# Kernel tuning notes

Hardware: AMD Instinct MI355X
Metric: run time of the kernel (lower is better)

## Reference

```python
import jax, jax.numpy as jnp
import numpy as np

N_NODES = 100000
N_EDGES = 1600000
N_GRAPHS = 64
D_IN, D_HID, D_OUT = 256, 128, 64
EPS = 1e-5


def gcn_conv(x, edge_index, edge_weight, W, b):
    """PyG GCNConv: add_self_loops=True, normalize=True (sym deg norm), bias."""
    n = x.shape[0]
    row = jnp.concatenate([edge_index[0], jnp.arange(n)])      # source
    col = jnp.concatenate([edge_index[1], jnp.arange(n)])      # target
    w = jnp.concatenate([edge_weight, jnp.ones((n,), x.dtype)])
    deg = jax.ops.segment_sum(w, col, num_segments=n)
    dinv = jnp.where(deg > 0, jax.lax.rsqrt(jnp.maximum(deg, EPS)), 0.0)
    norm = dinv[row] * w * dinv[col]                           # [E+N]
    h = x @ W                                                  # [N, out]
    msg = h[row] * norm[:, None]                               # [E+N, out]
    out = jax.ops.segment_sum(msg, col, num_segments=n)
    return out + b


def layer_norm(x, gamma, beta):
    mu = jnp.mean(x, axis=-1, keepdims=True)
    var = jnp.mean(jnp.square(x - mu), axis=-1, keepdims=True)
    return (x - mu) * jax.lax.rsqrt(var + EPS) * gamma + beta


def setup_inputs() -> dict:
    key = jax.random.key(0)
    ks = jax.random.split(key, 12)
    x = jax.random.normal(ks[0], (N_NODES, D_IN), jnp.float32)
    edge_index = jax.random.randint(ks[1], (2, N_EDGES), 0, N_NODES, jnp.int32)
    edge_weight = jax.random.uniform(ks[2], (N_EDGES,), jnp.float32)
    batch = jnp.sort(jax.random.randint(ks[3], (N_NODES,), 0, N_GRAPHS, jnp.int32))
    s1 = 1.0 / np.sqrt(D_IN)
    s2 = 1.0 / np.sqrt(D_HID)
    return {
        "x": x, "edge_index": edge_index, "edge_weight": edge_weight, "batch": batch,
        "W1": jax.random.uniform(ks[4], (D_IN, D_HID), jnp.float32, -s1, s1),
        "b1": jnp.zeros((D_HID,), jnp.float32),
        "g1": jnp.ones((D_HID,), jnp.float32),
        "bt1": jnp.zeros((D_HID,), jnp.float32),
        "W2": jax.random.uniform(ks[5], (D_HID, D_OUT), jnp.float32, -s2, s2),
        "b2": jnp.zeros((D_OUT,), jnp.float32),
        "g2": jnp.ones((D_OUT,), jnp.float32),
        "bt2": jnp.zeros((D_OUT,), jnp.float32),
    }


def reference(x, edge_index, edge_weight, batch, W1, b1, g1, bt1, W2, b2, g2, bt2):
    # ConvLayer 1: GCNConv -> relu -> LayerNorm(node)
    h = gcn_conv(x, edge_index, edge_weight, W1, b1)
    h = layer_norm(jax.nn.relu(h), g1, bt1)
    # dropout is identity in eval mode
    # ConvLayer 2
    h = gcn_conv(h, edge_index, edge_weight, W2, b2)
    h = layer_norm(jax.nn.relu(h), g2, bt2)
    # global mean pool over batch vector
    sums = jax.ops.segment_sum(h, batch, num_segments=N_GRAPHS)
    cnts = jax.ops.segment_sum(jnp.ones((h.shape[0],), h.dtype), batch, num_segments=N_GRAPHS)
    pooled = sums / jnp.maximum(cnts, 1.0)[:, None]
    return jax.nn.sigmoid(pooled)
```

## Files before the change

### kernel.cpp

```cpp
#include <hip/hip_runtime.h>
#include <cstdint>

#define EPSV 1e-5f

typedef __bf16 bf16x8 __attribute__((ext_vector_type(8)));
typedef __bf16 bf16x2 __attribute__((ext_vector_type(2)));
typedef float  f32x4  __attribute__((ext_vector_type(4)));
typedef unsigned long long u64;
typedef unsigned int u32;

#define NSB  512
#define BCAP 6144

__device__ __forceinline__ unsigned char f32_to_fp8(float x) {
    const int p = __builtin_amdgcn_cvt_pk_fp8_f32(x, x, 0, false);
    return (unsigned char)(p & 0xFF);
}

__global__ __launch_bounds__(256) void k_bh(const int* __restrict__ eic,
                                            u32* __restrict__ bhT,
                                            int E, int CH, int NBK) {
    __shared__ int h[400];
    for (int i = threadIdx.x; i < NBK; i += 256) h[i] = 0;
    __syncthreads();
    const int lo = blockIdx.x * CH;
    const int hi = min(E, lo + CH);
    for (int e = lo + threadIdx.x; e < hi; e += 256)
        atomicAdd(&h[eic[e] >> 8], 1);
    __syncthreads();
    for (int b = threadIdx.x; b < NBK; b += 256)
        bhT[b * NSB + blockIdx.x] = (u32)h[b];
}

__global__ __launch_bounds__(256) void k_bsum(const u32* __restrict__ bhT,
                                              u32* __restrict__ tot) {
    __shared__ u32 ws[4];
    const int b = blockIdx.x;
    const u32* p = bhT + (long)b * NSB;
    u32 s = p[threadIdx.x] + p[threadIdx.x + 256];
#pragma unroll
    for (int o = 32; o >= 1; o >>= 1) s += __shfl_xor(s, o);
    if ((threadIdx.x & 63) == 0) ws[threadIdx.x >> 6] = s;
    __syncthreads();
    if (threadIdx.x == 0) tot[b] = ws[0] + ws[1] + ws[2] + ws[3];
}

__global__ __launch_bounds__(256) void k_bscan2(const u32* __restrict__ tot,
                                                int* __restrict__ barr, int NBK) {
    __shared__ int carry;
    __shared__ int wsum[4];
    if (threadIdx.x == 0) carry = 0;
    __syncthreads();
    const int lane = threadIdx.x & 63, w = threadIdx.x >> 6;
    for (int base = 0; base < NBK; base += 256) {
        const int i = base + threadIdx.x;
        const int v = (i < NBK) ? (int)tot[i] : 0;
        int s = v;
#pragma unroll
        for (int o = 1; o < 64; o <<= 1) {
            const int t = __shfl_up(s, o);
            if (lane >= o) s += t;
        }
        if (lane == 63) wsum[w] = s;
        __syncthreads();
        int add = carry;
        for (int k = 0; k < w; ++k) add += wsum[k];
        const int t4 = wsum[0] + wsum[1] + wsum[2] + wsum[3];
        if (i < NBK) barr[i] = add + s - v;
        __syncthreads();
        if (threadIdx.x == 0) {
            carry += t4;
            if (base + 256 >= NBK) barr[NBK] = carry;
        }
        __syncthreads();
    }
}

__global__ __launch_bounds__(256) void k_bbase(const u32* __restrict__ bhT,
                                               const int* __restrict__ barr,
                                               u32* __restrict__ baseT) {
    __shared__ u32 wsum[4];
    const int b = blockIdx.x;
    const u32* p = bhT + (long)b * NSB;
    u32* q = baseT + (long)b * NSB;
    const int lane = threadIdx.x & 63, w = threadIdx.x >> 6;
    const u32 v0 = p[2 * threadIdx.x];
    const u32 v1 = p[2 * threadIdx.x + 1];
    const u32 pv = v0 + v1;
    u32 s = pv;
#pragma unroll
    for (int o = 1; o < 64; o <<= 1) {
        const u32 t = __shfl_up(s, o);
        if (lane >= o) s += t;
    }
    if (lane == 63) wsum[w] = s;
    __syncthreads();
    u32 add = (u32)barr[b];
    for (int k = 0; k < w; ++k) add += wsum[k];
    const u32 excl = add + s - pv;
    q[2 * threadIdx.x] = excl;
    q[2 * threadIdx.x + 1] = excl + v0;
}

__global__ __launch_bounds__(256) void k_bscat(const int* __restrict__ ei,
                                               const float* __restrict__ ew,
                                               const u32* __restrict__ baseT,
                                               u64* __restrict__ buck,
                                               int E, int CH, int NBK) {
    __shared__ u32 base[400];
    __shared__ u32 cur[400];
    for (int i = threadIdx.x; i < NBK; i += 256) {
        base[i] = baseT[i * NSB + blockIdx.x];
        cur[i] = 0;
    }
    __syncthreads();
    const int lo = blockIdx.x * CH;
    const int hi = min(E, lo + CH);
    for (int e = lo + threadIdx.x; e < hi; e += 256) {
        const int c = ei[E + e];
        const int r = ei[e];
        const int b = c >> 8;
        const u32 rk = atomicAdd(&cur[b], 1u);
        const u32 w16 = (u32)(ew[e] * 65535.0f + 0.5f);
        buck[base[b] + rk] = ((u64)(c & 255) << 33) | ((u64)r << 16) | (u64)w16;
    }
}

__global__ __launch_bounds__(256) void k_bucket(const u64* __restrict__ buck,
                                                const int* __restrict__ barr,
                                                u64* __restrict__ srt,
                                                int* __restrict__ cnt,
                                                int* __restrict__ off,
                                                float* __restrict__ dinv, int N) {
    __shared__ u64 arr[BCAP];
    __shared__ int lc[256];
    __shared__ float ldeg[256];
    __shared__ int loff[256];
    __shared__ int wsum[4];
    const int b = blockIdx.x;
    const int e0 = barr[b];
    const int nb = min(barr[b + 1] - e0, BCAP);

    lc[threadIdx.x] = 0;
    ldeg[threadIdx.x] = 0.f;
    __syncthreads();

    for (int i = threadIdx.x; i < nb; i += 256) {
        const u64 v = buck[e0 + i];
        arr[i] = v;
        const int cl = (int)(v >> 33) & 255;
        atomicAdd(&lc[cl], 1);
        atomicAdd(&ldeg[cl], (float)(u32)(v & 0xFFFF) * (1.0f / 65535.0f));
    }
    __syncthreads();

    const int lane = threadIdx.x & 63, w = threadIdx.x >> 6;
    const int vv = lc[threadIdx.x];
    int s = vv;
#pragma unroll
    for (int o = 1; o < 64; o <<= 1) {
        const int t = __shfl_up(s, o);
        if (lane >= o) s += t;
    }
    if (lane == 63) wsum[w] = s;
    __syncthreads();
    int add = 0;
    for (int k = 0; k < w; ++k) add += wsum[k];
    loff[threadIdx.x] = add + s - vv;
    __syncthreads();

    const int c = b * 256 + threadIdx.x;
    if (c < N) {
        cnt[c] = vv;
        off[c] = e0 + loff[threadIdx.x];
        dinv[c] = rsqrtf(1.0f + ldeg[threadIdx.x]);
    }

    __syncthreads();
    lc[threadIdx.x] = 0;
    __syncthreads();
    for (int i = threadIdx.x; i < nb; i += 256) {
        const u64 v = arr[i];
        const int cl = (int)(v >> 33) & 255;
        const int rk = atomicAdd(&lc[cl], 1);
        srt[e0 + loff[cl] + rk] =
            ((u64)(b * 256 + cl) << 33) | (v & 0x1FFFFFFFFull);
    }
}

__global__ __launch_bounds__(256) void k_norm(const u64* __restrict__ srt,
                                              const float* __restrict__ dinv,
                                              float2* __restrict__ ern, int E) {
    const int p = blockIdx.x * 256 + threadIdx.x;
    if (p >= E) return;
    const u64 v = srt[p];
    const int c = (int)(v >> 33);
    const int r = (int)((v >> 16) & 0x1FFFF);
    const float w = (float)(u32)(v & 0xFFFF) * (1.0f / 65535.0f);
    ern[p] = make_float2(__int_as_float(r), dinv[r] * w * dinv[c]);
}

__global__ __launch_bounds__(256) void k_wcvt(const float* __restrict__ W1,
                                              __bf16* __restrict__ Wt1,
                                              const float* __restrict__ W2,
                                              __bf16* __restrict__ Wt2) {
    const int idx = blockIdx.x * 256 + threadIdx.x;
    if (idx < 256 * 128) {
        const int k = idx >> 7, c = idx & 127;
        Wt1[(((k >> 3) << 7) + c) * 8 + (k & 7)] = (__bf16)W1[idx];
    } else if (idx < 256 * 128 + 128 * 64) {
        const int j = idx - 256 * 128;
        const int k = j >> 6, c = j & 63;
        Wt2[(((k >> 3) << 6) + c) * 8 + (k & 7)] = (__bf16)W2[j];
    }
}

template <int K, int NOUT, bool ABF16>
__device__ __forceinline__ void mm_body(int bid, int tid, const void* __restrict__ Xv,
                                        const __bf16* __restrict__ WtB,
                                        unsigned char* __restrict__ H, int N) {
    constexpr int NCB = NOUT / 16;
    constexpr int NKB = K / 32;
    const int w = tid >> 6, l = tid & 63;
    const int r0 = l & 15, kq = l >> 4;
    const long tb0 = (long)bid * 128 + w * 32;
    const long ar0 = (tb0 + r0) < N ? (tb0 + r0) : (long)N - 1;
    const long ar1 = (tb0 + 16 + r0) < N ? (tb0 + 16 + r0) : (long)N - 1;

    f32x4 acc[2][NCB];
#pragma unroll
    for (int rf = 0; rf < 2; ++rf)
#pragma unroll
        for (int cb = 0; cb < NCB; ++cb) acc[rf][cb] = (f32x4){0.f, 0.f, 0.f, 0.f};

#define LDA(kb, a0, a1)                                                          \
    {                                                                            \
        const int koff = (kb) * 32 + kq * 8;                                     \
        if constexpr (ABF16) {                                                   \
            a0 = *reinterpret_cast<const bf16x8*>((const __bf16*)Xv + ar0 * K + koff); \
            a1 = *reinterpret_cast<const bf16x8*>((const __bf16*)Xv + ar1 * K + koff); \
        } else {                                                                 \
            const float* p0 = (const float*)Xv + ar0 * K + koff;                 \
            const float* p1 = (const float*)Xv + ar1 * K + koff;                 \
            const float4 u0 = *reinterpret_cast<const float4*>(p0);              \
            const float4 u1 = *reinterpret_cast<const float4*>(p0 + 4);          \
            const float4 u2 = *reinterpret_cast<const float4*>(p1);              \
            const float4 u3 = *reinterpret_cast<const float4*>(p1 + 4);          \
            a0[0] = (__bf16)u0.x; a0[1] = (__bf16)u0.y; a0[2] = (__bf16)u0.z;    \
            a0[3] = (__bf16)u0.w; a0[4] = (__bf16)u1.x; a0[5] = (__bf16)u1.y;    \
            a0[6] = (__bf16)u1.z; a0[7] = (__bf16)u1.w;                          \
            a1[0] = (__bf16)u2.x; a1[1] = (__bf16)u2.y; a1[2] = (__bf16)u2.z;    \
            a1[3] = (__bf16)u2.w; a1[4] = (__bf16)u3.x; a1[5] = (__bf16)u3.y;    \
            a1[6] = (__bf16)u3.z; a1[7] = (__bf16)u3.w;                          \
        }                                                                        \
    }

#define LDB(kb, b)                                                               \
    {                                                                            \
        const __bf16* bp = WtB + (long)(((kb) * 4 + kq) * NOUT + r0) * 8;        \
        _Pragma("unroll") for (int cb = 0; cb < NCB; ++cb)                       \
            b[cb] = *reinterpret_cast<const bf16x8*>(bp + cb * 128);             \
    }

    bf16x8 aC0, aC1, aN0, aN1;
    bf16x8 bC[NCB], bN[NCB];
    LDA(0, aC0, aC1);
    LDB(0, bC);
#pragma unroll
    for (int kb = 0; kb < NKB; ++kb) {
        if (kb + 1 < NKB) {
            LDA(kb + 1, aN0, aN1);
            LDB(kb + 1, bN);
        }
#pragma unroll
        for (int cb = 0; cb < NCB; ++cb) {
            acc[0][cb] = __builtin_amdgcn_mfma_f32_16x16x32_bf16(aC0, bC[cb], acc[0][cb], 0, 0, 0);
            acc[1][cb] = __builtin_amdgcn_mfma_f32_16x16x32_bf16(aC1, bC[cb], acc[1][cb], 0, 0, 0);
        }
        aC0 = aN0; aC1 = aN1;
#pragma unroll
        for (int cb = 0; cb < NCB; ++cb) bC[cb] = bN[cb];
    }
#undef LDA
#undef LDB

    const int orow = kq * 4;
#pragma unroll
    for (int rf = 0; rf < 2; ++rf)
#pragma unroll
        for (int cb = 0; cb < NCB; ++cb)
#pragma unroll
            for (int r = 0; r < 4; ++r) {
                const long gr = tb0 + rf * 16 + orow + r;
                if (gr < N) H[gr * NOUT + cb * 16 + r0] = f32_to_fp8(acc[rf][cb][r]);
            }
}

__global__ __launch_bounds__(256) void k_mm1(const float* __restrict__ X,
                                             const __bf16* __restrict__ Wt1,
                                             unsigned char* __restrict__ H, int N) {
    mm_body<256, 128, false>(blockIdx.x, threadIdx.x, X, Wt1, H, N);
}

__global__ __launch_bounds__(256) void k_mm2(const __bf16* __restrict__ X,
                                             const __bf16* __restrict__ Wt2,
                                             unsigned char* __restrict__ H, int N) {
    mm_body<128, 64, true>(blockIdx.x, threadIdx.x, X, Wt2, H, N);
}

__global__ __launch_bounds__(256) void k_gat128(const unsigned char* __restrict__ H,
                                                const int* __restrict__ off,
                                                const int* __restrict__ cnt,
                                                const float2* __restrict__ ern,
                                                const float* __restrict__ dinv,
                                                const float* __restrict__ bias,
                                                const float* __restrict__ gm,
                                                const float* __restrict__ bt,
                                                __bf16* __restrict__ Out, int N) {
    const long wv = ((long)blockIdx.x * 256 + threadIdx.x) >> 6;
    const int lane = threadIdx.x & 63;
    if (wv >= N) return;
    const int s = off[wv];
    const int n = cnt[wv];
    const float d = dinv[wv];
    const unsigned short* Hp = reinterpret_cast<const unsigned short*>(H);

    const unsigned int h0 = Hp[wv * 64 + lane];
    float ax = __builtin_amdgcn_cvt_f32_fp8(h0, 0) * d * d;
    float ay = __builtin_amdgcn_cvt_f32_fp8(h0, 1) * d * d;

    int e = 0;
    for (; e + 8 <= n; e += 8) {
        float2 q[8];
#pragma unroll
        for (int j = 0; j < 8; ++j) q[j] = ern[s + e + j];
        unsigned int u[8];
#pragma unroll
        for (int j = 0; j < 8; ++j)
            u[j] = Hp[(long)__float_as_int(q[j].x) * 64 + lane];
#pragma unroll
        for (int j = 0; j < 8; ++j) {
            ax = fmaf(q[j].y, __builtin_amdgcn_cvt_f32_fp8(u[j], 0), ax);
            ay = fmaf(q[j].y, __builtin_amdgcn_cvt_f32_fp8(u[j], 1), ay);
        }
    }
    for (; e < n; ++e) {
        const float2 q = ern[s + e];
        const unsigned int u = Hp[(long)__float_as_int(q.x) * 64 + lane];
        ax = fmaf(q.y, __builtin_amdgcn_cvt_f32_fp8(u, 0), ax);
        ay = fmaf(q.y, __builtin_amdgcn_cvt_f32_fp8(u, 1), ay);
    }

    const float ux = fmaxf(ax + bias[2 * lane], 0.f);
    const float uy = fmaxf(ay + bias[2 * lane + 1], 0.f);
    float s1 = ux + uy, s2 = ux * ux + uy * uy;
#pragma unroll
    for (int o = 32; o >= 1; o >>= 1) {
        s1 += __shfl_xor(s1, o);
        s2 += __shfl_xor(s2, o);
    }
    const float mu = s1 * (1.f / 128.f);
    const float var = s2 * (1.f / 128.f) - mu * mu;
    const float rs = rsqrtf(var + EPSV);
    bf16x2 ob;
    ob[0] = (__bf16)((ux - mu) * rs * gm[2 * lane] + bt[2 * lane]);
    ob[1] = (__bf16)((uy - mu) * rs * gm[2 * lane + 1] + bt[2 * lane + 1]);
    reinterpret_cast<bf16x2*>(Out)[wv * 64 + lane] = ob;
}

__global__ __launch_bounds__(256) void k_gat64(const unsigned char* __restrict__ H,
                                               const int* __restrict__ off,
                                               const int* __restrict__ cnt,
                                               const float2* __restrict__ ern,
                                               const float* __restrict__ dinv,
                                               const float* __restrict__ bias,
                                               const float* __restrict__ gm,
                                               const float* __restrict__ bt,
                                               __bf16* __restrict__ Out, int N) {
    const long wv = ((long)blockIdx.x * 256 + threadIdx.x) >> 6;
    const int lane = threadIdx.x & 63;
    if (wv >= N) return;
    const int s = off[wv];
    const int n = cnt[wv];
    const float d = dinv[wv];

    float acc = __builtin_amdgcn_cvt_f32_fp8((unsigned int)H[wv * 64 + lane], 0) * d * d;
    int e = 0;
    for (; e + 8 <= n; e += 8) {
        float2 q[8];
#pragma unroll
        for (int j = 0; j < 8; ++j) q[j] = ern[s + e + j];
        unsigned int u[8];
#pragma unroll
        for (int j = 0; j < 8; ++j)
            u[j] = H[(long)__float_as_int(q[j].x) * 64 + lane];
#pragma unroll
        for (int j = 0; j < 8; ++j)
            acc = fmaf(q[j].y, __builtin_amdgcn_cvt_f32_fp8(u[j], 0), acc);
    }
    for (; e < n; ++e) {
        const float2 q = ern[s + e];
        const unsigned int u = H[(long)__float_as_int(q.x) * 64 + lane];
        acc = fmaf(q.y, __builtin_amdgcn_cvt_f32_fp8(u, 0), acc);
    }

    const float u = fmaxf(acc + bias[lane], 0.f);
    float s1 = u, s2 = u * u;
#pragma unroll
    for (int o = 32; o >= 1; o >>= 1) {
        s1 += __shfl_xor(s1, o);
        s2 += __shfl_xor(s2, o);
    }
    const float mu = s1 * (1.f / 64.f);
    const float var = s2 * (1.f / 64.f) - mu * mu;
    const float rs = rsqrtf(var + EPSV);
    Out[wv * 64 + lane] = (__bf16)((u - mu) * rs * gm[lane] + bt[lane]);
}

__global__ __launch_bounds__(256) void k_pool(const __bf16* __restrict__ C,
                                              const int* __restrict__ batch,
                                              float* __restrict__ pool,
                                              int N, int chunk) {
    const int wg = blockIdx.x * 4 + (threadIdx.x >> 6);
    const int lane = threadIdx.x & 63;
    long i = (long)wg * chunk;
    const long end = (i + chunk < (long)N) ? i + chunk : (long)N;
    if (i >= end) return;

    int cur = batch[i];
    float acc = 0.f;
    int cn = 0;
    while (i < end) {
        if (i + 8 <= end && batch[i + 7] == cur) {
            float v[8];
#pragma unroll
            for (int j = 0; j < 8; ++j) v[j] = (float)C[(i + j) * 64 + lane];
            acc += ((v[0] + v[1]) + (v[2] + v[3])) + ((v[4] + v[5]) + (v[6] + v[7]));
            cn += 8;
            i += 8;
            continue;
        }
        const int b = batch[i];
        if (b != cur) {
            unsafeAtomicAdd(&pool[cur * 64 + lane], acc);
            if (lane == 0) unsafeAtomicAdd(&pool[64 * 64 + cur], (float)cn);
            cur = b;
            acc = 0.f;
            cn = 0;
        }
        acc += (float)C[i * 64 + lane];
        ++cn;
        ++i;
    }
    unsafeAtomicAdd(&pool[cur * 64 + lane], acc);
    if (lane == 0) unsafeAtomicAdd(&pool[64 * 64 + cur], (float)cn);
}

__global__ __launch_bounds__(256) void k_final(const float* __restrict__ pool,
                                               float* __restrict__ out) {
    const int i = blockIdx.x * 256 + threadIdx.x;
    if (i < 4096) {
        const int g = i >> 6;
        const float cnt = fmaxf(pool[64 * 64 + g], 1.0f);
        const float v = pool[i] / cnt;
        out[i] = 1.f / (1.f + expf(-v));
    }
}

extern "C" void kernel_launch(void* const* d_in, const int* in_sizes, int n_in,
                              void* d_out, int out_size, void* d_ws, size_t ws_size,
                              hipStream_t stream) {
    const float* x   = (const float*)d_in[0];
    const int*   ei  = (const int*)d_in[1];
    const float* ew  = (const float*)d_in[2];
    const int*   bat = (const int*)d_in[3];
    const float* W1  = (const float*)d_in[4];
    const float* b1  = (const float*)d_in[5];
    const float* g1  = (const float*)d_in[6];
    const float* bt1 = (const float*)d_in[7];
    const float* W2  = (const float*)d_in[8];
    const float* b2  = (const float*)d_in[9];
    const float* g2  = (const float*)d_in[10];
    const float* bt2 = (const float*)d_in[11];
    const int N = in_sizes[3];
    const int E = in_sizes[2];
    const int NBK = (N + 255) >> 8;
    const int NBKp = (NBK + 2) & ~1;

    u64*    buck = (u64*)d_ws;
    u64*    srt  = buck + E;
    float2* ern  = (float2*)(srt + E);
    u32*    bhT  = (u32*)(ern + E);
    u32*    baseT= bhT + (long)NBKp * NSB;
    u32*    tot  = baseT + (long)NBKp * NSB;
    int*    barr = (int*)(tot + NBKp);
    unsigned char* Ah = (unsigned char*)(barr + NBK + 9);
    __bf16* Bh   = (__bf16*)(Ah + (long)N * 128);
    __bf16* Cb   = Bh + (long)N * 128;
    float*  dinv = (float*)(Cb + (long)N * 64);
    int*    cnt  = (int*)(dinv + N);
    int*    off  = cnt + N;
    __bf16* Wt1  = (__bf16*)(off + N);
    __bf16* Wt2  = Wt1 + 128 * 256;
    float*  pool = (float*)(Wt2 + 64 * 128);

    const int nbE = (E + 255) / 256;
    const int nbW = (int)(((long)N * 64 + 255) / 256);
    const int NBM = (N + 127) / 128;
    const int CH  = (E + NSB - 1) / NSB;

    hipMemsetAsync(pool, 0, (64 * 64 + 64) * sizeof(float), stream);
    k_wcvt<<<(256 * 128 + 128 * 64 + 255) / 256, 256, 0, stream>>>(W1, Wt1, W2, Wt2);

    k_bh<<<NSB, 256, 0, stream>>>(ei + E, bhT, E, CH, NBK);
    k_bsum<<<NBK, 256, 0, stream>>>(bhT, tot);
    k_bscan2<<<1, 256, 0, stream>>>(tot, barr, NBK);
    k_bbase<<<NBK, 256, 0, stream>>>(bhT, barr, baseT);
    k_bscat<<<NSB, 256, 0, stream>>>(ei, ew, baseT, buck, E, CH, NBK);
    k_bucket<<<NBK, 256, 0, stream>>>(buck, barr, srt, cnt, off, dinv, N);
    k_norm<<<nbE, 256, 0, stream>>>(srt, dinv, ern, E);

    k_mm1<<<NBM, 256, 0, stream>>>(x, Wt1, Ah, N);
    k_gat128<<<nbW, 256, 0, stream>>>(Ah, off, cnt, ern, dinv, b1, g1, bt1, Bh, N);

    k_mm2<<<NBM, 256, 0, stream>>>(Bh, Wt2, Ah, N);
    k_gat64<<<nbW, 256, 0, stream>>>(Ah, off, cnt, ern, dinv, b2, g2, bt2, Cb, N);

    const int chunk = (N + 1023) / 1024;
    k_pool<<<256, 256, 0, stream>>>(Cb, bat, pool, N, chunk);
    k_final<<<16, 256, 0, stream>>>(pool, (float*)d_out);
}
```

Before: 286.4 us.

## Fuse mean-pool into layer-2 gather, sub-sort edges by source, use packed fp8 converts

```diff
diff --git a/kernel.cpp b/kernel.cpp
--- a/kernel.cpp
+++ b/kernel.cpp
@@ -133,57 +133,68 @@
                                                 int* __restrict__ off,
                                                 float* __restrict__ dinv, int N) {
     __shared__ u64 arr[BCAP];
-    __shared__ int lc[256];
+    __shared__ int lc2[2048];
+    __shared__ int loff2[2048];
     __shared__ float ldeg[256];
-    __shared__ int loff[256];
     __shared__ int wsum[4];
-    const int b = blockIdx.x;
+    const int b = blockIdx.x, t = threadIdx.x;
     const int e0 = barr[b];
     const int nb = min(barr[b + 1] - e0, BCAP);
 
-    lc[threadIdx.x] = 0;
-    ldeg[threadIdx.x] = 0.f;
-    __syncthreads();
-
-    for (int i = threadIdx.x; i < nb; i += 256) {
+    for (int i = t; i < 2048; i += 256) lc2[i] = 0;
+    ldeg[t] = 0.f;
+    __syncthreads();
+
+    for (int i = t; i < nb; i += 256) {
         const u64 v = buck[e0 + i];
         arr[i] = v;
         const int cl = (int)(v >> 33) & 255;
-        atomicAdd(&lc[cl], 1);
+        const int r = (int)((v >> 16) & 0x1FFFF);
+        atomicAdd(&lc2[(cl << 3) | (r >> 14)], 1);
         atomicAdd(&ldeg[cl], (float)(u32)(v & 0xFFFF) * (1.0f / 65535.0f));
     }
     __syncthreads();
 
-    const int lane = threadIdx.x & 63, w = threadIdx.x >> 6;
-    const int vv = lc[threadIdx.x];
-    int s = vv;
+    int loc[8];
+    int s = 0;
+#pragma unroll
+    for (int j = 0; j < 8; ++j) { loc[j] = s; s += lc2[t * 8 + j]; }
+    const int lane = t & 63, w = t >> 6;
+    const int ps = s;
+    int sc = ps;
 #pragma unroll
     for (int o = 1; o < 64; o <<= 1) {
-        const int t = __shfl_up(s, o);
-        if (lane >= o) s += t;
-    }
-    if (lane == 63) wsum[w] = s;
+        const int tt = __shfl_up(sc, o);
+        if (lane >= o) sc += tt;
+    }
+    if (lane == 63) wsum[w] = sc;
     __syncthreads();
     int add = 0;
     for (int k = 0; k < w; ++k) add += wsum[k];
-    loff[threadIdx.x] = add + s - vv;
-    __syncthreads();
-
-    const int c = b * 256 + threadIdx.x;
+    const int tbase = add + sc - ps;
+#pragma unroll
+    for (int j = 0; j < 8; ++j) loff2[t * 8 + j] = tbase + loc[j];
+    __syncthreads();
+
+    const int c = b * 256 + t;
     if (c < N) {
-        cnt[c] = vv;
-        off[c] = e0 + loff[threadIdx.x];
-        dinv[c] = rsqrtf(1.0f + ldeg[threadIdx.x]);
-    }
-
-    __syncthreads();
-    lc[threadIdx.x] = 0;
-    __syncthreads();
-    for (int i = threadIdx.x; i < nb; i += 256) {
+        const int o0 = loff2[t << 3];
+        const int o1 = (t == 255) ? nb : loff2[(t + 1) << 3];
+        cnt[c] = o1 - o0;
+        off[c] = e0 + o0;
+        dinv[c] = rsqrtf(1.0f + ldeg[t]);
+    }
+
+    __syncthreads();
+    for (int i = t; i < 2048; i += 256) lc2[i] = 0;
+    __syncthreads();
+    for (int i = t; i < nb; i += 256) {
         const u64 v = arr[i];
         const int cl = (int)(v >> 33) & 255;
-        const int rk = atomicAdd(&lc[cl], 1);
-        srt[e0 + loff[cl] + rk] =
+        const int r = (int)((v >> 16) & 0x1FFFF);
+        const int cls = (cl << 3) | (r >> 14);
+        const int rk = atomicAdd(&lc2[cls], 1);
+        srt[e0 + loff2[cls] + rk] =
             ((u64)(b * 256 + cl) << 33) | (v & 0x1FFFFFFFFull);
     }
 }
@@ -326,8 +337,8 @@
     const unsigned short* Hp = reinterpret_cast<const unsigned short*>(H);
 
     const unsigned int h0 = Hp[wv * 64 + lane];
-    float ax = __builtin_amdgcn_cvt_f32_fp8(h0, 0) * d * d;
-    float ay = __builtin_amdgcn_cvt_f32_fp8(h0, 1) * d * d;
+    const auto h0v = __builtin_amdgcn_cvt_pk_f32_fp8((int)h0, false);
+    float ax = h0v[0] * d * d, ay = h0v[1] * d * d;
 
     int e = 0;
     for (; e + 8 <= n; e += 8) {
@@ -340,15 +351,17 @@
             u[j] = Hp[(long)__float_as_int(q[j].x) * 64 + lane];
 #pragma unroll
         for (int j = 0; j < 8; ++j) {
-            ax = fmaf(q[j].y, __builtin_amdgcn_cvt_f32_fp8(u[j], 0), ax);
-            ay = fmaf(q[j].y, __builtin_amdgcn_cvt_f32_fp8(u[j], 1), ay);
+            const auto v = __builtin_amdgcn_cvt_pk_f32_fp8((int)u[j], false);
+            ax = fmaf(q[j].y, v[0], ax);
+            ay = fmaf(q[j].y, v[1], ay);
         }
     }
     for (; e < n; ++e) {
         const float2 q = ern[s + e];
         const unsigned int u = Hp[(long)__float_as_int(q.x) * 64 + lane];
-        ax = fmaf(q.y, __builtin_amdgcn_cvt_f32_fp8(u, 0), ax);
-        ay = fmaf(q.y, __builtin_amdgcn_cvt_f32_fp8(u, 1), ay);
+        const auto v = __builtin_amdgcn_cvt_pk_f32_fp8((int)u, false);
+        ax = fmaf(q.y, v[0], ax);
+        ay = fmaf(q.y, v[1], ay);
     }
 
     const float ux = fmaxf(ax + bias[2 * lane], 0.f);
@@ -376,84 +389,74 @@
                                                const float* __restrict__ bias,
                                                const float* __restrict__ gm,
                                                const float* __restrict__ bt,
-                                               __bf16* __restrict__ Out, int N) {
+                                               const int* __restrict__ batch,
+                                               float* __restrict__ pool, int N) {
+    __shared__ float pv[4][64];
+    __shared__ int pg[4];
     const long wv = ((long)blockIdx.x * 256 + threadIdx.x) >> 6;
     const int lane = threadIdx.x & 63;
-    if (wv >= N) return;
-    const int s = off[wv];
-    const int n = cnt[wv];
-    const float d = dinv[wv];
-
-    float acc = __builtin_amdgcn_cvt_f32_fp8((unsigned int)H[wv * 64 + lane], 0) * d * d;
-    int e = 0;
-    for (; e + 8 <= n; e += 8) {
-        float2 q[8];
-#pragma unroll
-        for (int j = 0; j < 8; ++j) q[j] = ern[s + e + j];
-        unsigned int u[8];
-#pragma unroll
-        for (int j = 0; j < 8; ++j)
-            u[j] = H[(long)__float_as_int(q[j].x) * 64 + lane];
-#pragma unroll
-        for (int j = 0; j < 8; ++j)
-            acc = fmaf(q[j].y, __builtin_amdgcn_cvt_f32_fp8(u[j], 0), acc);
-    }
-    for (; e < n; ++e) {
-        const float2 q = ern[s + e];
-        const unsigned int u = H[(long)__float_as_int(q.x) * 64 + lane];
-        acc = fmaf(q.y, __builtin_amdgcn_cvt_f32_fp8(u, 0), acc);
-    }
-
-    const float u = fmaxf(acc + bias[lane], 0.f);
-    float s1 = u, s2 = u * u;
-#pragma unroll
-    for (int o = 32; o >= 1; o >>= 1) {
-        s1 += __shfl_xor(s1, o);
-        s2 += __shfl_xor(s2, o);
-    }
-    const float mu = s1 * (1.f / 64.f);
-    const float var = s2 * (1.f / 64.f) - mu * mu;
-    const float rs = rsqrtf(var + EPSV);
-    Out[wv * 64 + lane] = (__bf16)((u - mu) * rs * gm[lane] + bt[lane]);
-}
-
-__global__ __launch_bounds__(256) void k_pool(const __bf16* __restrict__ C,
-                                              const int* __restrict__ batch,
-                                              float* __restrict__ pool,
-                                              int N, int chunk) {
-    const int wg = blockIdx.x * 4 + (threadIdx.x >> 6);
-    const int lane = threadIdx.x & 63;
-    long i = (long)wg * chunk;
-    const long end = (i + chunk < (long)N) ? i + chunk : (long)N;
-    if (i >= end) return;
-
-    int cur = batch[i];
-    float acc = 0.f;
-    int cn = 0;
-    while (i < end) {
-        if (i + 8 <= end && batch[i + 7] == cur) {
-            float v[8];
-#pragma unroll
-            for (int j = 0; j < 8; ++j) v[j] = (float)C[(i + j) * 64 + lane];
-            acc += ((v[0] + v[1]) + (v[2] + v[3])) + ((v[4] + v[5]) + (v[6] + v[7]));
-            cn += 8;
-            i += 8;
-            continue;
-        }
-        const int b = batch[i];
-        if (b != cur) {
-            unsafeAtomicAdd(&pool[cur * 64 + lane], acc);
-            if (lane == 0) unsafeAtomicAdd(&pool[64 * 64 + cur], (float)cn);
-            cur = b;
-            acc = 0.f;
-            cn = 0;
-        }
-        acc += (float)C[i * 64 + lane];
-        ++cn;
-        ++i;
-    }
-    unsafeAtomicAdd(&pool[cur * 64 + lane], acc);
-    if (lane == 0) unsafeAtomicAdd(&pool[64 * 64 + cur], (float)cn);
+    const int w = (threadIdx.x >> 6) & 3;
+
+    float val = 0.f;
+    int g = -1;
+    if (wv < N) {
+        const int s = off[wv];
+        const int n = cnt[wv];
+        const float d = dinv[wv];
+        float acc = __builtin_amdgcn_cvt_f32_fp8((unsigned int)H[wv * 64 + lane], 0) * d * d;
+        int e = 0;
+        for (; e + 8 <= n; e += 8) {
+            float2 q[8];
+#pragma unroll
+            for (int j = 0; j < 8; ++j) q[j] = ern[s + e + j];
+            unsigned int u[8];
+#pragma unroll
+            for (int j = 0; j < 8; ++j)
+                u[j] = H[(long)__float_as_int(q[j].x) * 64 + lane];
+#pragma unroll
+            for (int j = 0; j < 8; ++j)
+                acc = fmaf(q[j].y, __builtin_amdgcn_cvt_f32_fp8(u[j], 0), acc);
+        }
+        for (; e < n; ++e) {
+            const float2 q = ern[s + e];
+            const unsigned int u = H[(long)__float_as_int(q.x) * 64 + lane];
+            acc = fmaf(q.y, __builtin_amdgcn_cvt_f32_fp8(u, 0), acc);
+        }
+        const float uu = fmaxf(acc + bias[lane], 0.f);
+        float s1 = uu, s2 = uu * uu;
+#pragma unroll
+        for (int o = 32; o >= 1; o >>= 1) {
+            s1 += __shfl_xor(s1, o);
+            s2 += __shfl_xor(s2, o);
+        }
+        const float mu = s1 * (1.f / 64.f);
+        const float var = s2 * (1.f / 64.f) - mu * mu;
+        const float rs = rsqrtf(var + EPSV);
+        val = (uu - mu) * rs * gm[lane] + bt[lane];
+        g = batch[wv];
+    }
+
+    pv[w][lane] = val;
+    if (lane == 0) pg[w] = g;
+    __syncthreads();
+
+    if (w == 0) {
+#pragma unroll
+        for (int a = 0; a < 4; ++a) {
+            const int ga = pg[a];
+            if (ga < 0) continue;
+            bool first = true;
+            for (int b2 = 0; b2 < a; ++b2)
+                if (pg[b2] == ga) first = false;
+            if (!first) continue;
+            float s = pv[a][lane];
+            int cc = 1;
+            for (int b2 = a + 1; b2 < 4; ++b2)
+                if (pg[b2] == ga) { s += pv[b2][lane]; ++cc; }
+            unsafeAtomicAdd(&pool[ga * 64 + lane], s);
+            if (lane == 0) unsafeAtomicAdd(&pool[64 * 64 + ga], (float)cc);
+        }
+    }
 }
 
 __global__ __launch_bounds__(256) void k_final(const float* __restrict__ pool,
@@ -496,8 +499,7 @@
     int*    barr = (int*)(tot + NBKp);
     unsigned char* Ah = (unsigned char*)(barr + NBK + 9);
     __bf16* Bh   = (__bf16*)(Ah + (long)N * 128);
-    __bf16* Cb   = Bh + (long)N * 128;
-    float*  dinv = (float*)(Cb + (long)N * 64);
+    float*  dinv = (float*)(Bh + (long)N * 128);
     int*    cnt  = (int*)(dinv + N);
     int*    off  = cnt + N;
     __bf16* Wt1  = (__bf16*)(off + N);
@@ -524,9 +526,7 @@
     k_gat128<<<nbW, 256, 0, stream>>>(Ah, off, cnt, ern, dinv, b1, g1, bt1, Bh, N);
 
     k_mm2<<<NBM, 256, 0, stream>>>(Bh, Wt2, Ah, N);
-    k_gat64<<<nbW, 256, 0, stream>>>(Ah, off, cnt, ern, dinv, b2, g2, bt2, Cb, N);
-
-    const int chunk = (N + 1023) / 1024;
-    k_pool<<<256, 256, 0, stream>>>(Cb, bat, pool, N, chunk);
+    k_gat64<<<nbW, 256, 0, stream>>>(Ah, off, cnt, ern, dinv, b2, g2, bt2, bat, pool, N);
+
     k_final<<<16, 256, 0, stream>>>(pool, (float*)d_out);
 }
```

Result: slower. 413.7 us (+44.5%).

## Split first matmul across CSR build kernels and fold edge norm into gathers

Applied to the files above, without the earlier changes.

```diff
diff --git a/kernel.cpp b/kernel.cpp
--- a/kernel.cpp
+++ b/kernel.cpp
@@ -15,204 +15,6 @@
 __device__ __forceinline__ unsigned char f32_to_fp8(float x) {
     const int p = __builtin_amdgcn_cvt_pk_fp8_f32(x, x, 0, false);
     return (unsigned char)(p & 0xFF);
-}
-
-__global__ __launch_bounds__(256) void k_bh(const int* __restrict__ eic,
-                                            u32* __restrict__ bhT,
-                                            int E, int CH, int NBK) {
-    __shared__ int h[400];
-    for (int i = threadIdx.x; i < NBK; i += 256) h[i] = 0;
-    __syncthreads();
-    const int lo = blockIdx.x * CH;
-    const int hi = min(E, lo + CH);
-    for (int e = lo + threadIdx.x; e < hi; e += 256)
-        atomicAdd(&h[eic[e] >> 8], 1);
-    __syncthreads();
-    for (int b = threadIdx.x; b < NBK; b += 256)
-        bhT[b * NSB + blockIdx.x] = (u32)h[b];
-}
-
-__global__ __launch_bounds__(256) void k_bsum(const u32* __restrict__ bhT,
-                                              u32* __restrict__ tot) {
-    __shared__ u32 ws[4];
-    const int b = blockIdx.x;
-    const u32* p = bhT + (long)b * NSB;
-    u32 s = p[threadIdx.x] + p[threadIdx.x + 256];
-#pragma unroll
-    for (int o = 32; o >= 1; o >>= 1) s += __shfl_xor(s, o);
-    if ((threadIdx.x & 63) == 0) ws[threadIdx.x >> 6] = s;
-    __syncthreads();
-    if (threadIdx.x == 0) tot[b] = ws[0] + ws[1] + ws[2] + ws[3];
-}
-
-__global__ __launch_bounds__(256) void k_bscan2(const u32* __restrict__ tot,
-                                                int* __restrict__ barr, int NBK) {
-    __shared__ int carry;
-    __shared__ int wsum[4];
-    if (threadIdx.x == 0) carry = 0;
-    __syncthreads();
-    const int lane = threadIdx.x & 63, w = threadIdx.x >> 6;
-    for (int base = 0; base < NBK; base += 256) {
-        const int i = base + threadIdx.x;
-        const int v = (i < NBK) ? (int)tot[i] : 0;
-        int s = v;
-#pragma unroll
-        for (int o = 1; o < 64; o <<= 1) {
-            const int t = __shfl_up(s, o);
-            if (lane >= o) s += t;
-        }
-        if (lane == 63) wsum[w] = s;
-        __syncthreads();
-        int add = carry;
-        for (int k = 0; k < w; ++k) add += wsum[k];
-        const int t4 = wsum[0] + wsum[1] + wsum[2] + wsum[3];
-        if (i < NBK) barr[i] = add + s - v;
-        __syncthreads();
-        if (threadIdx.x == 0) {
-            carry += t4;
-            if (base + 256 >= NBK) barr[NBK] = carry;
-        }
-        __syncthreads();
-    }
-}
-
-__global__ __launch_bounds__(256) void k_bbase(const u32* __restrict__ bhT,
-                                               const int* __restrict__ barr,
-                                               u32* __restrict__ baseT) {
-    __shared__ u32 wsum[4];
-    const int b = blockIdx.x;
-    const u32* p = bhT + (long)b * NSB;
-    u32* q = baseT + (long)b * NSB;
-    const int lane = threadIdx.x & 63, w = threadIdx.x >> 6;
-    const u32 v0 = p[2 * threadIdx.x];
-    const u32 v1 = p[2 * threadIdx.x + 1];
-    const u32 pv = v0 + v1;
-    u32 s = pv;
-#pragma unroll
-    for (int o = 1; o < 64; o <<= 1) {
-        const u32 t = __shfl_up(s, o);
-        if (lane >= o) s += t;
-    }
-    if (lane == 63) wsum[w] = s;
-    __syncthreads();
-    u32 add = (u32)barr[b];
-    for (int k = 0; k < w; ++k) add += wsum[k];
-    const u32 excl = add + s - pv;
-    q[2 * threadIdx.x] = excl;
-    q[2 * threadIdx.x + 1] = excl + v0;
-}
-
-__global__ __launch_bounds__(256) void k_bscat(const int* __restrict__ ei,
-                                               const float* __restrict__ ew,
-                                               const u32* __restrict__ baseT,
-                                               u64* __restrict__ buck,
-                                               int E, int CH, int NBK) {
-    __shared__ u32 base[400];
-    __shared__ u32 cur[400];
-    for (int i = threadIdx.x; i < NBK; i += 256) {
-        base[i] = baseT[i * NSB + blockIdx.x];
-        cur[i] = 0;
-    }
-    __syncthreads();
-    const int lo = blockIdx.x * CH;
-    const int hi = min(E, lo + CH);
-    for (int e = lo + threadIdx.x; e < hi; e += 256) {
-        const int c = ei[E + e];
-        const int r = ei[e];
-        const int b = c >> 8;
-        const u32 rk = atomicAdd(&cur[b], 1u);
-        const u32 w16 = (u32)(ew[e] * 65535.0f + 0.5f);
-        buck[base[b] + rk] = ((u64)(c & 255) << 33) | ((u64)r << 16) | (u64)w16;
-    }
-}
-
-__global__ __launch_bounds__(256) void k_bucket(const u64* __restrict__ buck,
-                                                const int* __restrict__ barr,
-                                                u64* __restrict__ srt,
-                                                int* __restrict__ cnt,
-                                                int* __restrict__ off,
-                                                float* __restrict__ dinv, int N) {
-    __shared__ u64 arr[BCAP];
-    __shared__ int lc[256];
-    __shared__ float ldeg[256];
-    __shared__ int loff[256];
-    __shared__ int wsum[4];
-    const int b = blockIdx.x;
-    const int e0 = barr[b];
-    const int nb = min(barr[b + 1] - e0, BCAP);
-
-    lc[threadIdx.x] = 0;
-    ldeg[threadIdx.x] = 0.f;
-    __syncthreads();
-
-    for (int i = threadIdx.x; i < nb; i += 256) {
-        const u64 v = buck[e0 + i];
-        arr[i] = v;
-        const int cl = (int)(v >> 33) & 255;
-        atomicAdd(&lc[cl], 1);
-        atomicAdd(&ldeg[cl], (float)(u32)(v & 0xFFFF) * (1.0f / 65535.0f));
-    }
-    __syncthreads();
-
-    const int lane = threadIdx.x & 63, w = threadIdx.x >> 6;
-    const int vv = lc[threadIdx.x];
-    int s = vv;
-#pragma unroll
-    for (int o = 1; o < 64; o <<= 1) {
-        const int t = __shfl_up(s, o);
-        if (lane >= o) s += t;
-    }
-    if (lane == 63) wsum[w] = s;
-    __syncthreads();
-    int add = 0;
-    for (int k = 0; k < w; ++k) add += wsum[k];
-    loff[threadIdx.x] = add + s - vv;
-    __syncthreads();
-
-    const int c = b * 256 + threadIdx.x;
-    if (c < N) {
-        cnt[c] = vv;
-        off[c] = e0 + loff[threadIdx.x];
-        dinv[c] = rsqrtf(1.0f + ldeg[threadIdx.x]);
-    }
-
-    __syncthreads();
-    lc[threadIdx.x] = 0;
-    __syncthreads();
-    for (int i = threadIdx.x; i < nb; i += 256) {
-        const u64 v = arr[i];
-        const int cl = (int)(v >> 33) & 255;
-        const int rk = atomicAdd(&lc[cl], 1);
-        srt[e0 + loff[cl] + rk] =
-            ((u64)(b * 256 + cl) << 33) | (v & 0x1FFFFFFFFull);
-    }
-}
-
-__global__ __launch_bounds__(256) void k_norm(const u64* __restrict__ srt,
-                                              const float* __restrict__ dinv,
-                                              float2* __restrict__ ern, int E) {
-    const int p = blockIdx.x * 256 + threadIdx.x;
-    if (p >= E) return;
-    const u64 v = srt[p];
-    const int c = (int)(v >> 33);
-    const int r = (int)((v >> 16) & 0x1FFFF);
-    const float w = (float)(u32)(v & 0xFFFF) * (1.0f / 65535.0f);
-    ern[p] = make_float2(__int_as_float(r), dinv[r] * w * dinv[c]);
-}
-
-__global__ __launch_bounds__(256) void k_wcvt(const float* __restrict__ W1,
-                                              __bf16* __restrict__ Wt1,
-                                              const float* __restrict__ W2,
-                                              __bf16* __restrict__ Wt2) {
-    const int idx = blockIdx.x * 256 + threadIdx.x;
-    if (idx < 256 * 128) {
-        const int k = idx >> 7, c = idx & 127;
-        Wt1[(((k >> 3) << 7) + c) * 8 + (k & 7)] = (__bf16)W1[idx];
-    } else if (idx < 256 * 128 + 128 * 64) {
-        const int j = idx - 256 * 128;
-        const int k = j >> 6, c = j & 63;
-        Wt2[(((k >> 3) << 6) + c) * 8 + (k & 7)] = (__bf16)W2[j];
-    }
 }
 
 template <int K, int NOUT, bool ABF16>
@@ -296,10 +98,205 @@
             }
 }
 
-__global__ __launch_bounds__(256) void k_mm1(const float* __restrict__ X,
-                                             const __bf16* __restrict__ Wt1,
-                                             unsigned char* __restrict__ H, int N) {
-    mm_body<256, 128, false>(blockIdx.x, threadIdx.x, X, Wt1, H, N);
+__global__ __launch_bounds__(256) void k_bh_mm(const int* __restrict__ eic,
+                                               u32* __restrict__ bhT,
+                                               int E, int CH, int NBK,
+                                               const float* __restrict__ X,
+                                               const __bf16* __restrict__ Wt1,
+                                               unsigned char* __restrict__ H1, int N) {
+    __shared__ int h[400];
+    if ((int)blockIdx.x >= NSB) {
+        mm_body<256, 128, false>((int)blockIdx.x - NSB, threadIdx.x, X, Wt1, H1, N);
+        return;
+    }
+    for (int i = threadIdx.x; i < NBK; i += 256) h[i] = 0;
+    __syncthreads();
+    const int lo = blockIdx.x * CH;
+    const int hi = min(E, lo + CH);
+    for (int e = lo + threadIdx.x; e < hi; e += 256)
+        atomicAdd(&h[eic[e] >> 8], 1);
+    __syncthreads();
+    for (int b = threadIdx.x; b < NBK; b += 256)
+        bhT[b * NSB + blockIdx.x] = (u32)h[b];
+}
+
+__global__ __launch_bounds__(256) void k_bsum(const u32* __restrict__ bhT,
+                                              u32* __restrict__ tot) {
+    __shared__ u32 ws[4];
+    const int b = blockIdx.x;
+    const u32* p = bhT + (long)b * NSB;
+    u32 s = p[threadIdx.x] + p[threadIdx.x + 256];
+#pragma unroll
+    for (int o = 32; o >= 1; o >>= 1) s += __shfl_xor(s, o);
+    if ((threadIdx.x & 63) == 0) ws[threadIdx.x >> 6] = s;
+    __syncthreads();
+    if (threadIdx.x == 0) tot[b] = ws[0] + ws[1] + ws[2] + ws[3];
+}
+
+__global__ __launch_bounds__(256) void k_bscan2(const u32* __restrict__ tot,
+                                                int* __restrict__ barr, int NBK) {
+    __shared__ int carry;
+    __shared__ int wsum[4];
+    if (threadIdx.x == 0) carry = 0;
+    __syncthreads();
+    const int lane = threadIdx.x & 63, w = threadIdx.x >> 6;
+    for (int base = 0; base < NBK; base += 256) {
+        const int i = base + threadIdx.x;
+        const int v = (i < NBK) ? (int)tot[i] : 0;
+        int s = v;
+#pragma unroll
+        for (int o = 1; o < 64; o <<= 1) {
+            const int t = __shfl_up(s, o);
+            if (lane >= o) s += t;
+        }
+        if (lane == 63) wsum[w] = s;
+        __syncthreads();
+        int add = carry;
+        for (int k = 0; k < w; ++k) add += wsum[k];
+        const int t4 = wsum[0] + wsum[1] + wsum[2] + wsum[3];
+        if (i < NBK) barr[i] = add + s - v;
+        __syncthreads();
+        if (threadIdx.x == 0) {
+            carry += t4;
+            if (base + 256 >= NBK) barr[NBK] = carry;
+        }
+        __syncthreads();
+    }
+}
+
+__global__ __launch_bounds__(256) void k_bbase(const u32* __restrict__ bhT,
+                                               const int* __restrict__ barr,
+                                               u32* __restrict__ baseT) {
+    __shared__ u32 wsum[4];
+    const int b = blockIdx.x;
+    const u32* p = bhT + (long)b * NSB;
+    u32* q = baseT + (long)b * NSB;
+    const int lane = threadIdx.x & 63, w = threadIdx.x >> 6;
+    const u32 v0 = p[2 * threadIdx.x];
+    const u32 v1 = p[2 * threadIdx.x + 1];
+    const u32 pv = v0 + v1;
+    u32 s = pv;
+#pragma unroll
+    for (int o = 1; o < 64; o <<= 1) {
+        const u32 t = __shfl_up(s, o);
+        if (lane >= o) s += t;
+    }
+    if (lane == 63) wsum[w] = s;
+    __syncthreads();
+    u32 add = (u32)barr[b];
+    for (int k = 0; k < w; ++k) add += wsum[k];
+    const u32 excl = add + s - pv;
+    q[2 * threadIdx.x] = excl;
+    q[2 * threadIdx.x + 1] = excl + v0;
+}
+
+__global__ __launch_bounds__(256) void k_bscat_mm(const int* __restrict__ ei,
+                                                  const float* __restrict__ ew,
+                                                  const u32* __restrict__ baseT,
+                                                  u64* __restrict__ buck,
+                                                  int E, int CH, int NBK,
+                                                  const float* __restrict__ X,
+                                                  const __bf16* __restrict__ Wt1,
+                                                  unsigned char* __restrict__ H1,
+                                                  int N, int P1) {
+    __shared__ u32 base[400];
+    __shared__ u32 cur[400];
+    if ((int)blockIdx.x >= NSB) {
+        mm_body<256, 128, false>(P1 + (int)blockIdx.x - NSB, threadIdx.x, X, Wt1, H1, N);
+        return;
+    }
+    for (int i = threadIdx.x; i < NBK; i += 256) {
+        base[i] = baseT[i * NSB + blockIdx.x];
+        cur[i] = 0;
+    }
+    __syncthreads();
+    const int lo = blockIdx.x * CH;
+    const int hi = min(E, lo + CH);
+    for (int e = lo + threadIdx.x; e < hi; e += 256) {
+        const int c = ei[E + e];
+        const int r = ei[e];
+        const int b = c >> 8;
+        const u32 rk = atomicAdd(&cur[b], 1u);
+        const u32 w16 = (u32)(ew[e] * 65535.0f + 0.5f);
+        buck[base[b] + rk] = ((u64)(c & 255) << 33) | ((u64)r << 16) | (u64)w16;
+    }
+}
+
+__global__ __launch_bounds__(256) void k_bucket(const u64* __restrict__ buck,
+                                                const int* __restrict__ barr,
+                                                u64* __restrict__ srt,
+                                                int* __restrict__ cnt,
+                                                int* __restrict__ off,
+                                                float* __restrict__ dinv, int N) {
+    __shared__ u64 arr[BCAP];
+    __shared__ int lc[256];
+    __shared__ float ldeg[256];
+    __shared__ int loff[256];
+    __shared__ int wsum[4];
+    const int b = blockIdx.x;
+    const int e0 = barr[b];
+    const int nb = min(barr[b + 1] - e0, BCAP);
+
+    lc[threadIdx.x] = 0;
+    ldeg[threadIdx.x] = 0.f;
+    __syncthreads();
+
+    for (int i = threadIdx.x; i < nb; i += 256) {
+        const u64 v = buck[e0 + i];
+        arr[i] = v;
+        const int cl = (int)(v >> 33) & 255;
+        atomicAdd(&lc[cl], 1);
+        atomicAdd(&ldeg[cl], (float)(u32)(v & 0xFFFF) * (1.0f / 65535.0f));
+    }
+    __syncthreads();
+
+    const int lane = threadIdx.x & 63, w = threadIdx.x >> 6;
+    const int vv = lc[threadIdx.x];
+    int s = vv;
+#pragma unroll
+    for (int o = 1; o < 64; o <<= 1) {
+        const int t = __shfl_up(s, o);
+        if (lane >= o) s += t;
+    }
+    if (lane == 63) wsum[w] = s;
+    __syncthreads();
+    int add = 0;
+    for (int k = 0; k < w; ++k) add += wsum[k];
+    loff[threadIdx.x] = add + s - vv;
+    __syncthreads();
+
+    const int c = b * 256 + threadIdx.x;
+    if (c < N) {
+        cnt[c] = vv;
+        off[c] = e0 + loff[threadIdx.x];
+        dinv[c] = rsqrtf(1.0f + ldeg[threadIdx.x]);
+    }
+
+    __syncthreads();
+    lc[threadIdx.x] = 0;
+    __syncthreads();
+    for (int i = threadIdx.x; i < nb; i += 256) {
+        const u64 v = arr[i];
+        const int cl = (int)(v >> 33) & 255;
+        const int rk = atomicAdd(&lc[cl], 1);
+        srt[e0 + loff[cl] + rk] =
+            ((u64)(b * 256 + cl) << 33) | (v & 0x1FFFFFFFFull);
+    }
+}
+
+__global__ __launch_bounds__(256) void k_wcvt(const float* __restrict__ W1,
+                                              __bf16* __restrict__ Wt1,
+                                              const float* __restrict__ W2,
+                                              __bf16* __restrict__ Wt2) {
+    const int idx = blockIdx.x * 256 + threadIdx.x;
+    if (idx < 256 * 128) {
+        const int k = idx >> 7, c = idx & 127;
+        Wt1[(((k >> 3) << 7) + c) * 8 + (k & 7)] = (__bf16)W1[idx];
+    } else if (idx < 256 * 128 + 128 * 64) {
+        const int j = idx - 256 * 128;
+        const int k = j >> 6, c = j & 63;
+        Wt2[(((k >> 3) << 6) + c) * 8 + (k & 7)] = (__bf16)W2[j];
+    }
 }
 
 __global__ __launch_bounds__(256) void k_mm2(const __bf16* __restrict__ X,
@@ -311,7 +308,7 @@
 __global__ __launch_bounds__(256) void k_gat128(const unsigned char* __restrict__ H,
                                                 const int* __restrict__ off,
                                                 const int* __restrict__ cnt,
-                                                const float2* __restrict__ ern,
+                                                const u64* __restrict__ srt,
                                                 const float* __restrict__ dinv,
                                                 const float* __restrict__ bias,
                                                 const float* __restrict__ gm,
@@ -323,32 +320,45 @@
     const int s = off[wv];
     const int n = cnt[wv];
     const float d = dinv[wv];
+    const float dd = d * (1.0f / 65535.0f);
     const unsigned short* Hp = reinterpret_cast<const unsigned short*>(H);
 
     const unsigned int h0 = Hp[wv * 64 + lane];
-    float ax = __builtin_amdgcn_cvt_f32_fp8(h0, 0) * d * d;
-    float ay = __builtin_amdgcn_cvt_f32_fp8(h0, 1) * d * d;
+    const auto h0v = __builtin_amdgcn_cvt_pk_f32_fp8((int)h0, false);
+    float ax = h0v[0] * d * d, ay = h0v[1] * d * d;
 
     int e = 0;
     for (; e + 8 <= n; e += 8) {
-        float2 q[8];
-#pragma unroll
-        for (int j = 0; j < 8; ++j) q[j] = ern[s + e + j];
+        long rj[8];
+        float wj[8];
+#pragma unroll
+        for (int j = 0; j < 8; ++j) {
+            const u64 v = srt[s + e + j];
+            rj[j] = (long)((v >> 16) & 0x1FFFF);
+            wj[j] = (float)(u32)(v & 0xFFFF);
+        }
         unsigned int u[8];
 #pragma unroll
-        for (int j = 0; j < 8; ++j)
-            u[j] = Hp[(long)__float_as_int(q[j].x) * 64 + lane];
+        for (int j = 0; j < 8; ++j) u[j] = Hp[rj[j] * 64 + lane];
+        float dv[8];
+#pragma unroll
+        for (int j = 0; j < 8; ++j) dv[j] = dinv[rj[j]];
 #pragma unroll
         for (int j = 0; j < 8; ++j) {
-            ax = fmaf(q[j].y, __builtin_amdgcn_cvt_f32_fp8(u[j], 0), ax);
-            ay = fmaf(q[j].y, __builtin_amdgcn_cvt_f32_fp8(u[j], 1), ay);
+            const float nr = dv[j] * wj[j] * dd;
+            const auto v = __builtin_amdgcn_cvt_pk_f32_fp8((int)u[j], false);
+            ax = fmaf(nr, v[0], ax);
+            ay = fmaf(nr, v[1], ay);
         }
     }
     for (; e < n; ++e) {
-        const float2 q = ern[s + e];
-        const unsigned int u = Hp[(long)__float_as_int(q.x) * 64 + lane];
-        ax = fmaf(q.y, __builtin_amdgcn_cvt_f32_fp8(u, 0), ax);
-        ay = fmaf(q.y, __builtin_amdgcn_cvt_f32_fp8(u, 1), ay);
+        const u64 vv = srt[s + e];
+        const long r = (long)((vv >> 16) & 0x1FFFF);
+        const float nr = dinv[r] * (float)(u32)(vv & 0xFFFF) * dd;
+        const unsigned int u = Hp[r * 64 + lane];
+        const auto v = __builtin_amdgcn_cvt_pk_f32_fp8((int)u, false);
+        ax = fmaf(nr, v[0], ax);
+        ay = fmaf(nr, v[1], ay);
     }
 
     const float ux = fmaxf(ax + bias[2 * lane], 0.f);
@@ -371,7 +381,7 @@
 __global__ __launch_bounds__(256) void k_gat64(const unsigned char* __restrict__ H,
                                                const int* __restrict__ off,
                                                const int* __restrict__ cnt,
-                                               const float2* __restrict__ ern,
+                                               const u64* __restrict__ srt,
                                                const float* __restrict__ dinv,
                                                const float* __restrict__ bias,
                                                const float* __restrict__ gm,
@@ -383,25 +393,34 @@
     const int s = off[wv];
     const int n = cnt[wv];
     const float d = dinv[wv];
+    const float dd = d * (1.0f / 65535.0f);
 
     float acc = __builtin_amdgcn_cvt_f32_fp8((unsigned int)H[wv * 64 + lane], 0) * d * d;
     int e = 0;
     for (; e + 8 <= n; e += 8) {
-        float2 q[8];
-#pragma unroll
-        for (int j = 0; j < 8; ++j) q[j] = ern[s + e + j];
+        long rj[8];
+        float wj[8];
+#pragma unroll
+        for (int j = 0; j < 8; ++j) {
+            const u64 v = srt[s + e + j];
+            rj[j] = (long)((v >> 16) & 0x1FFFF);
+            wj[j] = (float)(u32)(v & 0xFFFF);
+        }
         unsigned int u[8];
 #pragma unroll
+        for (int j = 0; j < 8; ++j) u[j] = H[rj[j] * 64 + lane];
+        float dv[8];
+#pragma unroll
+        for (int j = 0; j < 8; ++j) dv[j] = dinv[rj[j]];
+#pragma unroll
         for (int j = 0; j < 8; ++j)
-            u[j] = H[(long)__float_as_int(q[j].x) * 64 + lane];
-#pragma unroll
-        for (int j = 0; j < 8; ++j)
-            acc = fmaf(q[j].y, __builtin_amdgcn_cvt_f32_fp8(u[j], 0), acc);
+            acc = fmaf(dv[j] * wj[j] * dd, __builtin_amdgcn_cvt_f32_fp8(u[j], 0), acc);
     }
     for (; e < n; ++e) {
-        const float2 q = ern[s + e];
-        const unsigned int u = H[(long)__float_as_int(q.x) * 64 + lane];
-        acc = fmaf(q.y, __builtin_amdgcn_cvt_f32_fp8(u, 0), acc);
+        const u64 vv = srt[s + e];
+        const long r = (long)((vv >> 16) & 0x1FFFF);
+        const float nr = dinv[r] * (float)(u32)(vv & 0xFFFF) * dd;
+        acc = fmaf(nr, __builtin_amdgcn_cvt_f32_fp8((unsigned int)H[r * 64 + lane], 0), acc);
     }
 
     const float u = fmaxf(acc + bias[lane], 0.f);
@@ -489,8 +508,7 @@
 
     u64*    buck = (u64*)d_ws;
     u64*    srt  = buck + E;
-    float2* ern  = (float2*)(srt + E);
-    u32*    bhT  = (u32*)(ern + E);
+    u32*    bhT  = (u32*)(srt + E);
     u32*    baseT= bhT + (long)NBKp * NSB;
     u32*    tot  = baseT + (long)NBKp * NSB;
     int*    barr = (int*)(tot + NBKp);
@@ -504,27 +522,26 @@
     __bf16* Wt2  = Wt1 + 128 * 256;
     float*  pool = (float*)(Wt2 + 64 * 128);
 
-    const int nbE = (E + 255) / 256;
     const int nbW = (int)(((long)N * 64 + 255) / 256);
     const int NBM = (N + 127) / 128;
+    const int P1  = NBM / 2;
     const int CH  = (E + NSB - 1) / NSB;
 
     hipMemsetAsync(pool, 0, (64 * 64 + 64) * sizeof(float), stream);
     k_wcvt<<<(256 * 128 + 128 * 64 + 255) / 256, 256, 0, stream>>>(W1, Wt1, W2, Wt2);
 
-    k_bh<<<NSB, 256, 0, stream>>>(ei + E, bhT, E, CH, NBK);
+    k_bh_mm<<<NSB + P1, 256, 0, stream>>>(ei + E, bhT, E, CH, NBK, x, Wt1, Ah, N);
     k_bsum<<<NBK, 256, 0, stream>>>(bhT, tot);
     k_bscan2<<<1, 256, 0, stream>>>(tot, barr, NBK);
     k_bbase<<<NBK, 256, 0, stream>>>(bhT, barr, baseT);
-    k_bscat<<<NSB, 256, 0, stream>>>(ei, ew, baseT, buck, E, CH, NBK);
+    k_bscat_mm<<<NSB + (NBM - P1), 256, 0, stream>>>(ei, ew, baseT, buck, E, CH, NBK,
+                                                     x, Wt1, Ah, N, P1);
     k_bucket<<<NBK, 256, 0, stream>>>(buck, barr, srt, cnt, off, dinv, N);
-    k_norm<<<nbE, 256, 0, stream>>>(srt, dinv, ern, E);
-
-    k_mm1<<<NBM, 256, 0, stream>>>(x, Wt1, Ah, N);
-    k_gat128<<<nbW, 256, 0, stream>>>(Ah, off, cnt, ern, dinv, b1, g1, bt1, Bh, N);
+
+    k_gat128<<<nbW, 256, 0, stream>>>(Ah, off, cnt, srt, dinv, b1, g1, bt1, Bh, N);
 
     k_mm2<<<NBM, 256, 0, stream>>>(Bh, Wt2, Ah, N);
-    k_gat64<<<nbW, 256, 0, stream>>>(Ah, off, cnt, ern, dinv, b2, g2, bt2, Cb, N);
+    k_gat64<<<nbW, 256, 0, stream>>>(Ah, off, cnt, srt, dinv, b2, g2, bt2, Cb, N);
 
     const int chunk = (N + 1023) / 1024;
     k_pool<<<256, 256, 0, stream>>>(Cb, bat, pool, N, chunk);
```

Result: no change. 288.3 us (+0.7%).
